# Optimization experiments

Hardware: AMD Instinct MI355X
Metric: run time of the kernel (lower is better)

Reference implementation:

```python
import jax, jax.numpy as jnp
import numpy as np

EPS = 1e-12


def t5_layer_norm(x, w):
    # RMS norm without mean subtraction (T5 style)
    var = jnp.mean(x * x, axis=-1, keepdims=True)
    return w * (x * jax.lax.rsqrt(var + EPS))


def gether(h, a_simi, t_simi, adj):
    # h: [B,S,S,D]; a_simi/t_simi: [B,S]; adj: [B,S,S]
    diag = jnp.einsum('bssd->bsd', h)                 # h[b,l,l,:]
    h_adj = jnp.einsum('bld,blk->blkd', diag, adj)    # diag broadcast by adjacency
    h_y = h * t_simi[:, None, :, None]                # t_simi varies along axis 2
    h_x = h * a_simi[:, :, None, None]                # a_simi varies along axis 1
    h_left = jnp.pad(h_y, ((0, 0), (0, 0), (1, 0), (0, 0)))[:, :, :-1, :]
    h_right = jnp.pad(h_y, ((0, 0), (0, 0), (0, 1), (0, 0)))[:, :, 1:, :]
    h_up = jnp.pad(h_x, ((0, 0), (1, 0), (0, 0), (0, 0)))[:, :-1, :, :]
    h_down = jnp.pad(h_x, ((0, 0), (0, 1), (0, 0), (0, 0)))[:, 1:, :, :]
    return h + h_adj + h_left + h_right + h_up + h_down


def setup_inputs() -> dict:
    key = jax.random.key(0)
    ks = jax.random.split(key, 10)
    B, S, D_in, D_out = 8, 96, 768, 256
    table = jax.random.normal(ks[0], (B, S, S, D_in), dtype=jnp.float32)
    a_simi = jax.random.uniform(ks[1], (B, S), dtype=jnp.float32)
    t_simi = jax.random.uniform(ks[2], (B, S), dtype=jnp.float32)
    adj_matrix = jax.random.uniform(ks[3], (B, S, S), dtype=jnp.float32)
    s1 = 1.0 / np.sqrt(D_in)
    W1 = jax.random.uniform(ks[4], (D_in, D_in), jnp.float32, -s1, s1)
    b1 = jax.random.uniform(ks[5], (D_in,), jnp.float32, -s1, s1)
    g1 = jnp.ones((D_in,), jnp.float32)
    W2 = jax.random.uniform(ks[6], (D_in, D_out), jnp.float32, -s1, s1)
    b2 = jax.random.uniform(ks[7], (D_out,), jnp.float32, -s1, s1)
    g2 = jnp.ones((D_out,), jnp.float32)
    return {"table": table, "a_simi": a_simi, "t_simi": t_simi,
            "adj_matrix": adj_matrix, "W1": W1, "b1": b1, "g1": g1,
            "W2": W2, "b2": b2, "g2": g2}


def reference(table, a_simi, t_simi, adj_matrix, W1, b1, g1, W2, b2, g2):
    h0 = table
    h1 = gether(h0, a_simi, t_simi, adj_matrix)
    h1 = jax.nn.relu(t5_layer_norm((h1 + h0) @ W1 + b1, g1))
    h2 = gether(h1, a_simi, t_simi, adj_matrix)
    h2 = jax.nn.relu(t5_layer_norm((h2 + h1) @ W2 + b2, g2))
    return h2
```

## Files before the change

kernel.cpp:

```cpp
#include <hip/hip_runtime.h>

typedef __bf16 bf16;
typedef __bf16 bf16x4 __attribute__((ext_vector_type(4)));
typedef __bf16 bf16x8 __attribute__((ext_vector_type(8)));
typedef float f32x4 __attribute__((ext_vector_type(4)));
typedef float floatx4 __attribute__((ext_vector_type(4)));

#define S 96
#define DIN 768
#define DOUT 256
#define MROWS 73728

__device__ static inline void async16(const bf16* g, bf16* l) {
    __builtin_amdgcn_global_load_lds(
        (const __attribute__((address_space(1))) void*)g,
        (__attribute__((address_space(3))) void*)l,
        16, 0, 0);
}

__global__ __launch_bounds__(256) void k_gether1(
    const float* __restrict__ H, const float* __restrict__ Asim,
    const float* __restrict__ Tsim, const float* __restrict__ Adj,
    bf16* __restrict__ X)
{
    __shared__ float adjs[S];
    __shared__ float ts[S];
    __shared__ float diagf[DIN];
    int b = blockIdx.x / S, l = blockIdx.x % S;
    int tid = threadIdx.x;
    long row0 = (long)(b * S + l) * S;
    if (tid < S) {
        adjs[tid] = Adj[(b * S + l) * S + tid];
        ts[tid]   = Tsim[b * S + tid];
    }
    for (int i = tid; i < DIN / 4; i += 256)
        *(f32x4*)&diagf[i * 4] = *(const f32x4*)&H[(row0 + l) * DIN + i * 4];
    float a_up = (l > 0)     ? Asim[b * S + l - 1] : 0.f;
    float a_dn = (l < S - 1) ? Asim[b * S + l + 1] : 0.f;
    long du = (l > 0)     ? -(long)S * DIN : 0;
    long dd = (l < S - 1) ?  (long)S * DIN : 0;
    __syncthreads();

    for (int it = tid; it < S * (DIN / 4); it += 256) {
        int k = it / (DIN / 4);
        int c = it - k * (DIN / 4);
        const float* hc = H + (row0 + k) * DIN + c * 4;
        float tl = (k > 0)     ? ts[k - 1] : 0.f;
        float tr = (k < S - 1) ? ts[k + 1] : 0.f;
        long  dl = (k > 0)     ? -(long)DIN : 0;
        long  dr = (k < S - 1) ?  (long)DIN : 0;
        f32x4 vc = *(const f32x4*)hc;
        f32x4 vl = *(const f32x4*)(hc + dl);
        f32x4 vr = *(const f32x4*)(hc + dr);
        f32x4 vu = *(const f32x4*)(hc + du);
        f32x4 vd = *(const f32x4*)(hc + dd);
        float aj = adjs[k];
        bf16x4 o;
#pragma unroll
        for (int j = 0; j < 4; ++j) {
            float v = 2.f * vc[j] + aj * diagf[c * 4 + j]
                    + tl * vl[j] + tr * vr[j]
                    + a_up * vu[j] + a_dn * vd[j];
            o[j] = (bf16)v;
        }
        *(bf16x4*)&X[(row0 + k) * DIN + c * 4] = o;
    }
}

__global__ __launch_bounds__(256) void k_gether2(
    const bf16* __restrict__ Y, const float* __restrict__ INV,
    const float* __restrict__ G1, const float* __restrict__ Asim,
    const float* __restrict__ Tsim, const float* __restrict__ Adj,
    bf16* __restrict__ X)
{
    __shared__ float adjs[S];
    __shared__ float ts[S];
    __shared__ float diagf[DIN];
    __shared__ float g1s[DIN];
    int b = blockIdx.x / S, l = blockIdx.x % S;
    int tid = threadIdx.x;
    long row0 = (long)(b * S + l) * S;
    for (int i = tid; i < DIN; i += 256) g1s[i] = G1[i];
    __syncthreads();
    if (tid < S) {
        adjs[tid] = Adj[(b * S + l) * S + tid];
        ts[tid]   = Tsim[b * S + tid];
        float iv = INV[row0 + l];
        bf16x8 yv = *(const bf16x8*)&Y[(row0 + l) * DIN + tid * 8];
#pragma unroll
        for (int j = 0; j < 8; ++j) {
            float v = g1s[tid * 8 + j] * (float)yv[j] * iv;
            diagf[tid * 8 + j] = v > 0.f ? v : 0.f;
        }
    }
    float a_up = (l > 0)     ? Asim[b * S + l - 1] : 0.f;
    float a_dn = (l < S - 1) ? Asim[b * S + l + 1] : 0.f;
    long du = (l > 0)     ? -(long)S * DIN : 0;
    long dd = (l < S - 1) ?  (long)S * DIN : 0;
    int ou = (l > 0) ? -S : 0;
    int od = (l < S - 1) ? S : 0;
    __syncthreads();

    for (int it = tid; it < S * (DIN / 8); it += 256) {
        int k = it / (DIN / 8);
        int c = it - k * (DIN / 8);
        const bf16* yc = Y + (row0 + k) * DIN + c * 8;
        float tl = (k > 0)     ? ts[k - 1] : 0.f;
        float tr = (k < S - 1) ? ts[k + 1] : 0.f;
        int   ol = (k > 0)     ? -1 : 0;
        int   orr = (k < S - 1) ? 1 : 0;
        float ivc = INV[row0 + k];
        float ivl = INV[row0 + k + ol];
        float ivr = INV[row0 + k + orr];
        float ivu = INV[row0 + k + ou];
        float ivd = INV[row0 + k + od];
        bf16x8 vc = *(const bf16x8*)yc;
        bf16x8 vl = *(const bf16x8*)(yc + (long)ol * DIN);
        bf16x8 vr = *(const bf16x8*)(yc + (long)orr * DIN);
        bf16x8 vu = *(const bf16x8*)(yc + du);
        bf16x8 vd = *(const bf16x8*)(yc + dd);
        float aj = adjs[k];
        bf16x8 o;
#pragma unroll
        for (int j = 0; j < 8; ++j) {
            float g = g1s[c * 8 + j];
            float hc_ = g * (float)vc[j] * ivc; hc_ = hc_ > 0.f ? hc_ : 0.f;
            float hl_ = g * (float)vl[j] * ivl; hl_ = hl_ > 0.f ? hl_ : 0.f;
            float hr_ = g * (float)vr[j] * ivr; hr_ = hr_ > 0.f ? hr_ : 0.f;
            float hu_ = g * (float)vu[j] * ivu; hu_ = hu_ > 0.f ? hu_ : 0.f;
            float hd_ = g * (float)vd[j] * ivd; hd_ = hd_ > 0.f ? hd_ : 0.f;
            float v = 2.f * hc_ + aj * diagf[c * 8 + j]
                    + tl * hl_ + tr * hr_ + a_up * hu_ + a_dn * hd_;
            o[j] = (bf16)v;
        }
        *(bf16x8*)&X[(row0 + k) * DIN + c * 8] = o;
    }
}

template <int N, typename OutT>
__global__ __launch_bounds__(256) void k_gemm(
    const bf16* __restrict__ Xm, const bf16* __restrict__ WT,
    const float* __restrict__ bias, OutT* __restrict__ Y,
    float* __restrict__ ssq)
{
    constexpr int K = 768;
    __shared__ __align__(16) bf16 As[128 * 32];
    __shared__ __align__(16) bf16 Bs[128 * 32];
    int t = threadIdx.x;
    int colBase = blockIdx.x * 128;
    int rowBase = blockIdx.y * 128;
    int lane = t & 63, w = t >> 6;
    int quad = lane >> 4, l16 = lane & 15;
    int wr = w >> 1, wc = w & 1;

    floatx4 acc[4][4];
#pragma unroll
    for (int i = 0; i < 4; ++i)
#pragma unroll
        for (int j = 0; j < 4; ++j) acc[i][j] = (floatx4)0.f;

    const bf16* gA = Xm + (size_t)(rowBase + (t >> 2)) * K + (t & 3) * 8;
    const bf16* gB = WT + (size_t)(colBase + (t >> 2)) * K + (t & 3) * 8;
    bf16* ldsA = &As[t * 8];
    bf16* ldsB = &Bs[t * 8];

    for (int kk = 0; kk < K; kk += 32) {
        __syncthreads();
        async16(gA + kk, ldsA);
        async16(gA + kk + 64 * K, ldsA + 2048);
        async16(gB + kk, ldsB);
        async16(gB + kk + 64 * K, ldsB + 2048);
        __syncthreads();
        bf16x8 af[4], bfr[4];
#pragma unroll
        for (int i = 0; i < 4; ++i)
            af[i] = *(const bf16x8*)&As[(wr * 64 + i * 16 + l16) * 32 + quad * 8];
#pragma unroll
        for (int i = 0; i < 4; ++i)
            bfr[i] = *(const bf16x8*)&Bs[(wc * 64 + i * 16 + l16) * 32 + quad * 8];
#pragma unroll
        for (int i = 0; i < 4; ++i)
#pragma unroll
            for (int j = 0; j < 4; ++j)
                acc[i][j] = __builtin_amdgcn_mfma_f32_16x16x32_bf16(
                    af[i], bfr[j], acc[i][j], 0, 0, 0);
    }

    float bv[4];
#pragma unroll
    for (int j = 0; j < 4; ++j)
        bv[j] = bias[colBase + wc * 64 + j * 16 + l16];
#pragma unroll
    for (int i = 0; i < 4; ++i) {
#pragma unroll
        for (int r = 0; r < 4; ++r) {
            int row = rowBase + wr * 64 + i * 16 + quad * 4 + r;
            OutT* yp = Y + (size_t)row * N + colBase + wc * 64 + l16;
            float s = 0.f;
#pragma unroll
            for (int j = 0; j < 4; ++j) {
                float v = acc[i][j][r] + bv[j];
                s += v * v;
                yp[j * 16] = (OutT)v;
            }
            s += __shfl_xor(s, 1);
            s += __shfl_xor(s, 2);
            s += __shfl_xor(s, 4);
            s += __shfl_xor(s, 8);
            if (l16 == 0) atomicAdd(&ssq[row], s);
        }
    }
}

__global__ __launch_bounds__(256) void k_invr(float* ssq, int n, float invD)
{
    int i = blockIdx.x * 256 + threadIdx.x;
    if (i < n) ssq[i] = rsqrtf(ssq[i] * invD + 1e-12f);
}

__global__ __launch_bounds__(256) void k_final(
    const float* __restrict__ Y2, const float* __restrict__ ssq2,
    const float* __restrict__ G2, float* __restrict__ out)
{
    int gidx = blockIdx.x * 256 + threadIdx.x;
    int r = gidx >> 6;
    int c = (gidx & 63) * 4;
    float inv = rsqrtf(ssq2[r] * (1.f / DOUT) + 1e-12f);
    f32x4 yv = *(const f32x4*)&Y2[(size_t)r * DOUT + c];
    f32x4 o;
#pragma unroll
    for (int j = 0; j < 4; ++j) {
        float v = G2[c + j] * yv[j] * inv;
        o[j] = v > 0.f ? v : 0.f;
    }
    *(f32x4*)&out[(size_t)r * DOUT + c] = o;
}

__global__ __launch_bounds__(256) void k_castT(
    const float* __restrict__ in, bf16* __restrict__ out, int R, int C)
{
    int idx = blockIdx.x * 256 + threadIdx.x;
    if (idx < R * C) {
        int c = idx / R, r = idx - c * R;
        out[idx] = (bf16)in[r * C + c];
    }
}

extern "C" void kernel_launch(void* const* d_in, const int* in_sizes, int n_in,
                              void* d_out, int out_size, void* d_ws, size_t ws_size,
                              hipStream_t stream)
{
    const float* table = (const float*)d_in[0];
    const float* asim  = (const float*)d_in[1];
    const float* tsim  = (const float*)d_in[2];
    const float* adj   = (const float*)d_in[3];
    const float* W1    = (const float*)d_in[4];
    const float* b1    = (const float*)d_in[5];
    const float* g1    = (const float*)d_in[6];
    const float* W2    = (const float*)d_in[7];
    const float* b2    = (const float*)d_in[8];
    const float* g2    = (const float*)d_in[9];
    float* out = (float*)d_out;

    char* ws = (char*)d_ws;
    const size_t SZ_X = (size_t)MROWS * DIN * 2;
    bf16*  X    = (bf16*)ws;
    bf16*  Y1   = (bf16*)(ws + SZ_X);
    float* Y2   = (float*)(ws + SZ_X);
    bf16*  W1T  = (bf16*)(ws + 2 * SZ_X);
    bf16*  W2T  = (bf16*)(ws + 2 * SZ_X + 1179648);
    float* ssq1 = (float*)(ws + 2 * SZ_X + 1179648 + 393216);
    float* ssq2 = ssq1 + MROWS;

    hipMemsetAsync(ssq1, 0, (size_t)MROWS * 4 * 2, stream);
    k_castT<<<2304, 256, 0, stream>>>(W1, W1T, DIN, DIN);
    k_castT<<<768, 256, 0, stream>>>(W2, W2T, DIN, DOUT);

    k_gether1<<<8 * S, 256, 0, stream>>>(table, asim, tsim, adj, X);
    k_gemm<DIN, bf16><<<dim3(DIN / 128, MROWS / 128), 256, 0, stream>>>(X, W1T, b1, Y1, ssq1);
    k_invr<<<MROWS / 256, 256, 0, stream>>>(ssq1, MROWS, 1.f / DIN);
    k_gether2<<<8 * S, 256, 0, stream>>>(Y1, ssq1, g1, asim, tsim, adj, X);
    k_gemm<DOUT, float><<<dim3(DOUT / 128, MROWS / 128), 256, 0, stream>>>(X, W2T, b2, Y2, ssq2);
    k_final<<<(MROWS * DOUT / 4) / 256, 256, 0, stream>>>(Y2, ssq2, g2, out);
}
```

Before: 700.3 us.

## Swizzle GEMM LDS layout, widen GEMM1 tile to 192 cols, tile weight transpose

Both GEMMs now XOR-swizzle the 16-byte chunk position in LDS, on both the async global-to-LDS store and the MFMA fragment reads, to reduce LDS bank conflicts. GEMM1 uses a 128x192 tile (6 MFMA column fragments per wave) so each A tile is reused across more columns and fewer A reloads occur. Both GEMM grids now put the row-block index in x instead of y, which changes the order blocks run in and how the weight tile is reused in cache. The weight cast-transpose now goes through a 32x33 shared-memory tile for coalesced access; this is a small, one-off cost. The wider tile raises accumulator register use and may lower occupancy.

```diff
diff --git a/kernel.cpp b/kernel.cpp
--- a/kernel.cpp
+++ b/kernel.cpp
@@ -137,18 +137,97 @@
     }
 }
 
-template <int N, typename OutT>
-__global__ __launch_bounds__(256) void k_gemm(
+__global__ __launch_bounds__(256) void k_gemm1(
     const bf16* __restrict__ Xm, const bf16* __restrict__ WT,
-    const float* __restrict__ bias, OutT* __restrict__ Y,
+    const float* __restrict__ bias, bf16* __restrict__ Y,
     float* __restrict__ ssq)
 {
-    constexpr int K = 768;
+    constexpr int K = 768, N = 768;
+    __shared__ __align__(16) bf16 As[128 * 32];
+    __shared__ __align__(16) bf16 Bs[192 * 32];
+    int t = threadIdx.x;
+    int rowBase = blockIdx.x * 128;
+    int colBase = blockIdx.y * 192;
+    int lane = t & 63, w = t >> 6;
+    int quad = lane >> 4, l16 = lane & 15;
+    int wr = w >> 1, wc = w & 1;
+
+    floatx4 acc[4][6];
+#pragma unroll
+    for (int i = 0; i < 4; ++i)
+#pragma unroll
+        for (int j = 0; j < 6; ++j) acc[i][j] = (floatx4)0.f;
+
+    int chunk = (t & 3) ^ ((t >> 3) & 3);
+    const bf16* gA = Xm + (size_t)(rowBase + (t >> 2)) * K + chunk * 8;
+    const bf16* gB = WT + (size_t)(colBase + (t >> 2)) * K + chunk * 8;
+    bf16* ldsA = &As[t * 8];
+    bf16* ldsB = &Bs[t * 8];
+
+    for (int kk = 0; kk < K; kk += 32) {
+        __syncthreads();
+        async16(gA + kk, ldsA);
+        async16(gA + kk + 64 * K, ldsA + 2048);
+        async16(gB + kk, ldsB);
+        async16(gB + kk + 64 * K, ldsB + 2048);
+        async16(gB + kk + 128 * K, ldsB + 4096);
+        __syncthreads();
+        bf16x8 af[4], bfr[6];
+#pragma unroll
+        for (int i = 0; i < 4; ++i) {
+            int ra = wr * 64 + i * 16 + l16;
+            af[i] = *(const bf16x8*)&As[ra * 32 + (quad ^ ((ra >> 1) & 3)) * 8];
+        }
+#pragma unroll
+        for (int j = 0; j < 6; ++j) {
+            int rb = wc * 96 + j * 16 + l16;
+            bfr[j] = *(const bf16x8*)&Bs[rb * 32 + (quad ^ ((rb >> 1) & 3)) * 8];
+        }
+#pragma unroll
+        for (int i = 0; i < 4; ++i)
+#pragma unroll
+            for (int j = 0; j < 6; ++j)
+                acc[i][j] = __builtin_amdgcn_mfma_f32_16x16x32_bf16(
+                    af[i], bfr[j], acc[i][j], 0, 0, 0);
+    }
+
+    float bv[6];
+#pragma unroll
+    for (int j = 0; j < 6; ++j)
+        bv[j] = bias[colBase + wc * 96 + j * 16 + l16];
+#pragma unroll
+    for (int i = 0; i < 4; ++i) {
+#pragma unroll
+        for (int r = 0; r < 4; ++r) {
+            int row = rowBase + wr * 64 + i * 16 + quad * 4 + r;
+            bf16* yp = Y + (size_t)row * N + colBase + wc * 96 + l16;
+            float s = 0.f;
+#pragma unroll
+            for (int j = 0; j < 6; ++j) {
+                float v = acc[i][j][r] + bv[j];
+                s += v * v;
+                yp[j * 16] = (bf16)v;
+            }
+            s += __shfl_xor(s, 1);
+            s += __shfl_xor(s, 2);
+            s += __shfl_xor(s, 4);
+            s += __shfl_xor(s, 8);
+            if (l16 == 0) atomicAdd(&ssq[row], s);
+        }
+    }
+}
+
+__global__ __launch_bounds__(256) void k_gemm2(
+    const bf16* __restrict__ Xm, const bf16* __restrict__ WT,
+    const float* __restrict__ bias, float* __restrict__ Y,
+    float* __restrict__ ssq)
+{
+    constexpr int K = 768, N = 256;
     __shared__ __align__(16) bf16 As[128 * 32];
     __shared__ __align__(16) bf16 Bs[128 * 32];
     int t = threadIdx.x;
-    int colBase = blockIdx.x * 128;
-    int rowBase = blockIdx.y * 128;
+    int rowBase = blockIdx.x * 128;
+    int colBase = blockIdx.y * 128;
     int lane = t & 63, w = t >> 6;
     int quad = lane >> 4, l16 = lane & 15;
     int wr = w >> 1, wc = w & 1;
@@ -159,8 +238,9 @@
 #pragma unroll
         for (int j = 0; j < 4; ++j) acc[i][j] = (floatx4)0.f;
 
-    const bf16* gA = Xm + (size_t)(rowBase + (t >> 2)) * K + (t & 3) * 8;
-    const bf16* gB = WT + (size_t)(colBase + (t >> 2)) * K + (t & 3) * 8;
+    int chunk = (t & 3) ^ ((t >> 3) & 3);
+    const bf16* gA = Xm + (size_t)(rowBase + (t >> 2)) * K + chunk * 8;
+    const bf16* gB = WT + (size_t)(colBase + (t >> 2)) * K + chunk * 8;
     bf16* ldsA = &As[t * 8];
     bf16* ldsB = &Bs[t * 8];
 
@@ -173,11 +253,15 @@
         __syncthreads();
         bf16x8 af[4], bfr[4];
 #pragma unroll
-        for (int i = 0; i < 4; ++i)
-            af[i] = *(const bf16x8*)&As[(wr * 64 + i * 16 + l16) * 32 + quad * 8];
-#pragma unroll
-        for (int i = 0; i < 4; ++i)
-            bfr[i] = *(const bf16x8*)&Bs[(wc * 64 + i * 16 + l16) * 32 + quad * 8];
+        for (int i = 0; i < 4; ++i) {
+            int ra = wr * 64 + i * 16 + l16;
+            af[i] = *(const bf16x8*)&As[ra * 32 + (quad ^ ((ra >> 1) & 3)) * 8];
+        }
+#pragma unroll
+        for (int j = 0; j < 4; ++j) {
+            int rb = wc * 64 + j * 16 + l16;
+            bfr[j] = *(const bf16x8*)&Bs[rb * 32 + (quad ^ ((rb >> 1) & 3)) * 8];
+        }
 #pragma unroll
         for (int i = 0; i < 4; ++i)
 #pragma unroll
@@ -195,13 +279,13 @@
 #pragma unroll
         for (int r = 0; r < 4; ++r) {
             int row = rowBase + wr * 64 + i * 16 + quad * 4 + r;
-            OutT* yp = Y + (size_t)row * N + colBase + wc * 64 + l16;
+            float* yp = Y + (size_t)row * N + colBase + wc * 64 + l16;
             float s = 0.f;
 #pragma unroll
             for (int j = 0; j < 4; ++j) {
                 float v = acc[i][j][r] + bv[j];
                 s += v * v;
-                yp[j * 16] = (OutT)v;
+                yp[j * 16] = v;
             }
             s += __shfl_xor(s, 1);
             s += __shfl_xor(s, 2);
@@ -239,11 +323,16 @@
 __global__ __launch_bounds__(256) void k_castT(
     const float* __restrict__ in, bf16* __restrict__ out, int R, int C)
 {
-    int idx = blockIdx.x * 256 + threadIdx.x;
-    if (idx < R * C) {
-        int c = idx / R, r = idx - c * R;
-        out[idx] = (bf16)in[r * C + c];
-    }
+    __shared__ float tile[32][33];
+    int lx = threadIdx.x & 31, ly = threadIdx.x >> 5;
+    int c0 = blockIdx.x * 32, r0 = blockIdx.y * 32;
+#pragma unroll
+    for (int k = 0; k < 4; ++k)
+        tile[ly + 8 * k][lx] = in[(size_t)(r0 + ly + 8 * k) * C + c0 + lx];
+    __syncthreads();
+#pragma unroll
+    for (int k = 0; k < 4; ++k)
+        out[(size_t)(c0 + ly + 8 * k) * R + r0 + lx] = (bf16)tile[lx][ly + 8 * k];
 }
 
 extern "C" void kernel_launch(void* const* d_in, const int* in_sizes, int n_in,
@@ -273,13 +362,13 @@
     float* ssq2 = ssq1 + MROWS;
 
     hipMemsetAsync(ssq1, 0, (size_t)MROWS * 4 * 2, stream);
-    k_castT<<<2304, 256, 0, stream>>>(W1, W1T, DIN, DIN);
-    k_castT<<<768, 256, 0, stream>>>(W2, W2T, DIN, DOUT);
+    k_castT<<<dim3(DIN / 32, DIN / 32), 256, 0, stream>>>(W1, W1T, DIN, DIN);
+    k_castT<<<dim3(DOUT / 32, DIN / 32), 256, 0, stream>>>(W2, W2T, DIN, DOUT);
 
     k_gether1<<<8 * S, 256, 0, stream>>>(table, asim, tsim, adj, X);
-    k_gemm<DIN, bf16><<<dim3(DIN / 128, MROWS / 128), 256, 0, stream>>>(X, W1T, b1, Y1, ssq1);
+    k_gemm1<<<dim3(MROWS / 128, DIN / 192), 256, 0, stream>>>(X, W1T, b1, Y1, ssq1);
     k_invr<<<MROWS / 256, 256, 0, stream>>>(ssq1, MROWS, 1.f / DIN);
     k_gether2<<<8 * S, 256, 0, stream>>>(Y1, ssq1, g1, asim, tsim, adj, X);
-    k_gemm<DOUT, float><<<dim3(DOUT / 128, MROWS / 128), 256, 0, stream>>>(X, W2T, b2, Y2, ssq2);
+    k_gemm2<<<dim3(MROWS / 128, DOUT / 128), 256, 0, stream>>>(X, W2T, b2, Y2, ssq2);
     k_final<<<(MROWS * DOUT / 4) / 256, 256, 0, stream>>>(Y2, ssq2, g2, out);
 }
```

Measured after the change: 693.6 us. Within noise of the previous version (-1.0%).
